# Optimization experiments

Hardware: AMD Instinct MI355X
Metric: run time of the kernel (lower is better)

The kernel has to match this reference:

```python
import jax, jax.numpy as jnp
import numpy as np

B, CIN, L, D, H, DK, DV, K, KE = 8, 16, 256, 256, 8, 32, 32, 3, 5
EPS = 1e-9

def r2c(p):
    return p[..., 0] + 1j * p[..., 1]

def c2r(z):
    return jnp.stack([jnp.real(z), jnp.imag(z)], axis=-1)

def conv1d(x, w):
    # x: [B,C,L] complex, w: [O,C,Kt] complex, 'same' padding (pad = K//2)
    kt = w.shape[-1]; pad = kt // 2; Lx = x.shape[-1]
    xp = jnp.pad(x, ((0, 0), (0, 0), (pad, pad)))
    return sum(jnp.einsum('bcl,oc->bol', xp[:, :, i:i + Lx], w[:, :, i]) for i in range(kt))

def eca(x, w):
    # Efficient Channel Attention (complex): global avg pool over length,
    # 1D conv (kernel KE) across channels, split sigmoid gate, rescale.
    C = x.shape[1]; pad = w.shape[0] // 2
    y = x.mean(axis=-1)                              # [B,C] complex
    yp = jnp.pad(y, ((0, 0), (pad, pad)))
    z = sum(w[i] * yp[:, i:i + C] for i in range(w.shape[0]))
    a = jax.nn.sigmoid(z.real) + 1j * jax.nn.sigmoid(z.imag)
    return x * a[:, :, None]

def magminmax(s):
    # MagMinMaxNorm: min-max normalize magnitudes along last dim, keep phase.
    mag = jnp.abs(s)
    mn = mag.min(axis=-1, keepdims=True)
    mx = mag.max(axis=-1, keepdims=True)
    return s * (((mag - mn) / (mx - mn + EPS)) / (mag + EPS))

def mha(qi, ki, vi, Wq, Wk, Wv, Wo):
    # qi/ki/vi: [B, L, D] complex
    b, lq, _ = qi.shape
    q = jnp.einsum('bld,de->ble', qi, Wq).reshape(b, lq, H, DK)
    k = jnp.einsum('bld,de->ble', ki, Wk).reshape(b, -1, H, DK)
    v = jnp.einsum('bld,de->ble', vi, Wv).reshape(b, -1, H, DV)
    s = jnp.einsum('bqhd,bkhd->bhqk', q, k) * (1.0 / DK ** 0.5)
    o = jnp.einsum('bhqk,bkhd->bqhd', magminmax(s), v).reshape(b, lq, H * DV)
    return jnp.einsum('ble,ed->bld', o, Wo)

def ssca(A, Bx, Wq, Wk, Wv, Wo, eca_w, conv_w):
    # A, Bx: [B, D, L] complex. Wq/Wk/Wv/Wo indexed [AA, BB, AB, BA].
    At = jnp.swapaxes(A, 1, 2)
    Bt = jnp.swapaxes(Bx, 1, 2)
    Waa = mha(At, At, At, Wq[0], Wk[0], Wv[0], Wo[0])
    Xbb = mha(Bt, Bt, Bt, Wq[1], Wk[1], Wv[1], Wo[1])
    Yab = mha(At, Bt, Bt, Wq[2], Wk[2], Wv[2], Wo[2])
    Zba = mha(Bt, At, At, Wq[3], Wk[3], Wv[3], Wo[3])
    # cat along sequence dim (dim=1 pre-transpose in torch), then back to [B, D, 4L]
    Xc = jnp.swapaxes(jnp.concatenate([Waa, Xbb, Yab, Zba], axis=1), 1, 2)
    return conv1d(eca(Xc, eca_w), conv_w)

def fusion(X1, X2, head_w, head_b, wq, wk, wv, wo, ssca_eca_w, ssca_conv_w, top_eca_w):
    X1c, X2c = r2c(X1), r2c(X2)
    hw, hb = r2c(head_w), r2c(head_b)
    Wq, Wk, Wv, Wo = r2c(wq), r2c(wk), r2c(wv), r2c(wo)
    se, sc, te = r2c(ssca_eca_w), r2c(ssca_conv_w), r2c(top_eca_w)
    A = conv1d(X1c, hw[0]) + hb[0][None, :, None]
    Bc = conv1d(X2c, hw[1]) + hb[1][None, :, None]
    R = ssca(A, Bc, Wq[0], Wk[0], Wv[0], Wo[0], se[0], sc[0])
    kk = ssca(jnp.fft.ifft(A, axis=-1), jnp.fft.ifft(Bc, axis=-1),
              Wq[1], Wk[1], Wv[1], Wo[1], se[1], sc[1])
    R2 = jnp.concatenate([R, jnp.fft.fft(kk, axis=-1)], axis=1)      # [B, 2D, 4L]
    k2 = jnp.concatenate([kk, jnp.fft.ifft(R2[:, :D], axis=-1)], axis=1)
    return eca(R2, te[0]), eca(k2, te[1])

def setup_inputs() -> dict:
    key = jax.random.key(0)
    ks = jax.random.split(key, 11)
    def rn(k, shape, s=1.0):
        return jax.random.normal(k, shape, dtype=jnp.float32) * s
    wscale = 1.0 / D ** 0.5
    return {
        'X1': rn(ks[0], (B, CIN, L, 2)),
        'X2': rn(ks[1], (B, CIN, L, 2)),
        'head_w': rn(ks[2], (2, D, CIN, K, 2), 0.1),
        'head_b': rn(ks[3], (2, D, 2), 0.1),
        'wq': rn(ks[4], (2, 4, D, H * DK, 2), wscale),
        'wk': rn(ks[5], (2, 4, D, H * DK, 2), wscale),
        'wv': rn(ks[6], (2, 4, D, H * DV, 2), wscale),
        'wo': rn(ks[7], (2, 4, H * DV, D, 2), wscale),
        'ssca_eca_w': rn(ks[8], (2, KE, 2), 0.3),
        'ssca_conv_w': rn(ks[9], (2, D, D, K, 2), wscale),
        'top_eca_w': rn(ks[10], (2, KE, 2), 0.3),
    }

def reference(X1, X2, head_w, head_b, wq, wk, wv, wo, ssca_eca_w, ssca_conv_w, top_eca_w):
    Rc, kc = fusion(X1, X2, head_w, head_b, wq, wk, wv, wo, ssca_eca_w, ssca_conv_w, top_eca_w)
    return c2r(Rc), c2r(kc)
```

## Files before the change

kernel.cpp:

```cpp
#include <hip/hip_runtime.h>
#include <math.h>

namespace {

constexpr int Bn = 8, CINn = 16, Ln = 256, Dn = 256, Hn = 8, DKn = 32, DVn = 32;
constexpr int KWn = 3, KEn = 5, L4n = 1024;
constexpr float EPSf = 1e-9f;
constexpr int XP = 1040;
constexpr int LP = 40;

typedef __attribute__((ext_vector_type(8))) short short8b;
typedef __attribute__((ext_vector_type(4))) float f32x4;

__device__ __forceinline__ float2 cmul(float2 a, float2 b){
  return make_float2(a.x*b.x - a.y*b.y, a.x*b.y + a.y*b.x);
}
__device__ __forceinline__ float2 cfma(float2 a, float2 b, float2 c){
  c.x = fmaf(a.x, b.x, c.x); c.x = fmaf(-a.y, b.y, c.x);
  c.y = fmaf(a.x, b.y, c.y); c.y = fmaf(a.y, b.x, c.y);
  return c;
}
__device__ __forceinline__ ushort f2bf(float f){
  uint u = __float_as_uint(f);
  u += 0x7fffu + ((u >> 16) & 1u);
  return (ushort)(u >> 16);
}
__device__ __forceinline__ uint cvt_pk_bf16(float a, float b){
  uint u;
  asm("v_cvt_pk_bf16_f32 %0, %1, %2" : "=v"(u) : "v"(a), "v"(b));
  return u;
}
__device__ __forceinline__ short8b neg8(short8b v){
  union { short8b s; uint u[4]; } x; x.s = v;
  #pragma unroll
  for (int i = 0; i < 4; ++i) x.u[i] ^= 0x80008000u;
  return x.s;
}

__global__ void head_conv_kernel(const float2* __restrict__ X, const float2* __restrict__ hw,
                                 const float2* __restrict__ hb, float2* __restrict__ out){
  int idx = blockIdx.x * blockDim.x + threadIdx.x;
  if (idx >= Bn*Dn*Ln) return;
  int l = idx & (Ln-1);
  int o = (idx >> 8) & (Dn-1);
  int b = idx >> 16;
  float2 acc = hb[o];
  for (int c = 0; c < CINn; ++c){
    const float2* xr = X + (size_t)(b*CINn + c)*Ln;
    const float2* wr = hw + (size_t)(o*CINn + c)*KWn;
    #pragma unroll
    for (int i = 0; i < KWn; ++i){
      int ll = l + i - 1;
      if (ll >= 0 && ll < Ln) acc = cfma(xr[ll], wr[i], acc);
    }
  }
  out[idx] = acc;
}

template<int N, int LOG>
__global__ void fft_rows_kernel(const float2* __restrict__ src0, float2* __restrict__ dst0,
                                int schans, int scoff, int dchans, int dcoff,
                                float sign, float scale, float2* __restrict__ ysum){
  __shared__ float2 buf[N];
  __shared__ float2 tw[N/2];
  __shared__ float rx[256], ry[256];
  int row = blockIdx.x;
  int rb = row >> 8, rc = row & 255;
  const float2* src = src0 + (size_t)(rb*schans + scoff + rc)*N;
  float2* dst = dst0 + (size_t)(rb*dchans + dcoff + rc)*N;
  int tid = threadIdx.x;
  for (int i = tid; i < N/2; i += 256){
    float a = sign * 6.2831853071795864f * (float)i / (float)N;
    float s, c; __sincosf(a, &s, &c);
    tw[i] = make_float2(c, s);
  }
  for (int i = tid; i < N; i += 256){
    unsigned r = __brev((unsigned)i) >> (32 - LOG);
    buf[r] = src[i];
  }
  __syncthreads();
  for (int st = 1; st <= LOG; ++st){
    int half = 1 << (st-1);
    for (int bf = tid; bf < N/2; bf += 256){
      int blk = bf >> (st-1);
      int pos = bf & (half-1);
      int i0 = (blk << st) + pos;
      int i1 = i0 + half;
      float2 w = tw[pos << (LOG-st)];
      float2 u = buf[i0];
      float2 t = cmul(w, buf[i1]);
      buf[i0] = make_float2(u.x + t.x, u.y + t.y);
      buf[i1] = make_float2(u.x - t.x, u.y - t.y);
    }
    __syncthreads();
  }
  float sx = 0.f, sy = 0.f;
  for (int i = tid; i < N; i += 256){
    float2 o = make_float2(buf[i].x * scale, buf[i].y * scale);
    dst[i] = o; sx += o.x; sy += o.y;
  }
  if (ysum){
    rx[tid] = sx; ry[tid] = sy; __syncthreads();
    for (int st = 128; st > 0; st >>= 1){
      if (tid < st){ rx[tid] += rx[tid+st]; ry[tid] += ry[tid+st]; }
      __syncthreads();
    }
    if (tid == 0)
      ysum[(size_t)rb*dchans + dcoff + rc] = make_float2(rx[0]*(1.f/N), ry[0]*(1.f/N));
  }
}

__global__ void row_mean_map(const float2* __restrict__ src0, int schans, int scoff,
                             float2* __restrict__ y, int dchans, int dcoff){
  int row = blockIdx.x;
  int rb = row >> 8, rc = row & 255;
  const float2* xr = src0 + (size_t)(rb*schans + scoff + rc)*L4n;
  int tid = threadIdx.x;
  float sx = 0.f, sy = 0.f;
  for (int i = tid; i < L4n; i += 256){ float2 v = xr[i]; sx += v.x; sy += v.y; }
  __shared__ float rx[256], ry[256];
  rx[tid] = sx; ry[tid] = sy; __syncthreads();
  for (int st = 128; st > 0; st >>= 1){
    if (tid < st){ rx[tid] += rx[tid+st]; ry[tid] += ry[tid+st]; }
    __syncthreads();
  }
  if (tid == 0)
    y[(size_t)rb*dchans + dcoff + rc] = make_float2(rx[0]*(1.f/L4n), ry[0]*(1.f/L4n));
}

__device__ __forceinline__ void cgemm_core(
    const ushort* __restrict__ Are, const ushort* __restrict__ Aim, int pitchA, int am0,
    const ushort* __restrict__ Bre, const ushort* __restrict__ Bim, int pitchB, int n0,
    int K, int conv, float2* __restrict__ cbase, size_t crow, int cmode,
    ushort* __restrict__ ore, ushort* __restrict__ oim)
{
  __shared__ ushort sh[16896];
  ushort* As_re = sh;
  ushort* As_im = sh + 5120;
  ushort* Bs_re = sh + 10240;
  ushort* Bs_im = sh + 12800;
  int tid = threadIdx.x;
  int lane = tid & 63, w = tid >> 6;
  int lrow = lane & 15, lhalf = lane >> 4;
  f32x4 ar[2][4], ai[2][4];
  #pragma unroll
  for (int s = 0; s < 2; ++s)
    #pragma unroll
    for (int t = 0; t < 4; ++t){ ar[s][t] = (f32x4){0,0,0,0}; ai[s][t] = (f32x4){0,0,0,0}; }
  int nk = K >> 5;
  for (int kc = 0; kc < nk; ++kc){
    int k0 = kc << 5;
    __syncthreads();
    #pragma unroll
    for (int rep = 0; rep < 4; ++rep){
      int q = tid + rep*256;
      int row = q >> 3, kq = (q & 7)*4;
      size_t go = (size_t)(am0 + row)*pitchA + k0 + kq;
      *(uint2*)&As_re[row*LP + kq] = *(const uint2*)&Are[go];
      *(uint2*)&As_im[row*LP + kq] = *(const uint2*)&Aim[go];
    }
    if (!conv){
      #pragma unroll
      for (int rep = 0; rep < 2; ++rep){
        int q = tid + rep*256;
        int row = q >> 3, kq = (q & 7)*4;
        size_t go = (size_t)(n0 + row)*pitchB + k0 + kq;
        *(uint2*)&Bs_re[row*LP + kq] = *(const uint2*)&Bre[go];
        *(uint2*)&Bs_im[row*LP + kq] = *(const uint2*)&Bim[go];
      }
    } else {
      #pragma unroll
      for (int rep = 0; rep < 8; ++rep){
        int idx = tid + rep*256;
        int k = idx >> 6, nn = idx & 63;
        uint kk = (uint)(k0 + k);
        uint c = (kk * 0xAAABu) >> 17;
        int i = (int)(kk - c*3u);
        size_t go = (size_t)c*XP + 8 + n0 + nn + i - 1;
        Bs_re[nn*LP + k] = Bre[go];
        Bs_im[nn*LP + k] = Bim[go];
      }
    }
    __syncthreads();
    short8b afr[2], afi[2], bfr[4], bfi[4];
    #pragma unroll
    for (int s = 0; s < 2; ++s){
      int row = w*32 + s*16 + lrow;
      afr[s] = *(const short8b*)&As_re[row*LP + lhalf*8];
      afi[s] = *(const short8b*)&As_im[row*LP + lhalf*8];
    }
    #pragma unroll
    for (int t = 0; t < 4; ++t){
      int row = t*16 + lrow;
      bfr[t] = *(const short8b*)&Bs_re[row*LP + lhalf*8];
      bfi[t] = *(const short8b*)&Bs_im[row*LP + lhalf*8];
    }
    #pragma unroll
    for (int s = 0; s < 2; ++s){
      short8b ain = neg8(afi[s]);
      #pragma unroll
      for (int t = 0; t < 4; ++t){
        ar[s][t] = __builtin_amdgcn_mfma_f32_16x16x32_bf16(ain,    bfi[t], ar[s][t], 0, 0, 0);
        ar[s][t] = __builtin_amdgcn_mfma_f32_16x16x32_bf16(afr[s], bfr[t], ar[s][t], 0, 0, 0);
        ai[s][t] = __builtin_amdgcn_mfma_f32_16x16x32_bf16(afi[s], bfr[t], ai[s][t], 0, 0, 0);
        ai[s][t] = __builtin_amdgcn_mfma_f32_16x16x32_bf16(afr[s], bfi[t], ai[s][t], 0, 0, 0);
      }
    }
  }
  if (cmode == 0){
    #pragma unroll
    for (int s = 0; s < 2; ++s)
      #pragma unroll
      for (int t = 0; t < 4; ++t)
        #pragma unroll
        for (int r = 0; r < 4; ++r){
          int mm = w*32 + s*16 + lhalf*4 + r;
          int nn = t*16 + lrow;
          if (ore){
            ore[(size_t)mm*crow + nn] = f2bf(ar[s][t][r]);
            oim[(size_t)mm*crow + nn] = f2bf(ai[s][t][r]);
          } else {
            cbase[(size_t)mm*crow + nn] = make_float2(ar[s][t][r], ai[s][t][r]);
          }
        }
  } else {
    float2* T = (float2*)sh;
    #pragma unroll
    for (int h2 = 0; h2 < 2; ++h2){
      __syncthreads();
      #pragma unroll
      for (int s = 0; s < 2; ++s)
        #pragma unroll
        for (int t2 = 0; t2 < 2; ++t2){
          int t = h2*2 + t2;
          #pragma unroll
          for (int r = 0; r < 4; ++r){
            int mm = w*32 + s*16 + lhalf*4 + r;
            int nn = t2*16 + lrow;
            T[mm*33 + nn] = make_float2(ar[s][t][r], ai[s][t][r]);
          }
        }
      __syncthreads();
      #pragma unroll
      for (int rep = 0; rep < 16; ++rep){
        int idx = tid + rep*256;
        int mm = idx & 127, nn = idx >> 7;
        float2 v = T[mm*33 + nn];
        if (ore){
          ore[(size_t)(h2*32 + nn)*crow + mm] = f2bf(v.x);
          oim[(size_t)(h2*32 + nn)*crow + mm] = f2bf(v.y);
        } else {
          cbase[(size_t)(h2*32 + nn)*crow + mm] = v;
        }
      }
    }
  }
}

__global__ __launch_bounds__(256) void qkv_mfma(
    const ushort* __restrict__ aAre, const ushort* __restrict__ aAim,
    const ushort* __restrict__ aBre, const ushort* __restrict__ aBim,
    const ushort* __restrict__ WqRe, const ushort* __restrict__ WqIm,
    const ushort* __restrict__ WkRe, const ushort* __restrict__ WkIm,
    const ushort* __restrict__ WvRe, const ushort* __restrict__ WvIm,
    ushort* __restrict__ QpRe, ushort* __restrict__ QpIm,
    ushort* __restrict__ KpRe, ushort* __restrict__ KpIm,
    ushort* __restrict__ VpRe, ushort* __restrict__ VpIm,
    int set, int m0, size_t pstride)
{
  int my = blockIdx.y;
  int ml = my / 3, which = my - ml*3;
  int m = m0 + ml;
  bool useA = (which == 0) ? (m == 0 || m == 2) : (m == 0 || m == 3);
  const ushort* Are = useA ? aAre : aBre;
  const ushort* Aim = useA ? aAim : aBim;
  const ushort* WRe = (which == 0) ? WqRe : (which == 1) ? WkRe : WvRe;
  const ushort* WIm = (which == 0) ? WqIm : (which == 1) ? WkIm : WvIm;
  size_t woff = (size_t)(set*4 + m)*Dn*Dn;
  int bx = blockIdx.x;
  int nt = bx & 3, mt = (bx >> 2) & 1, b = bx >> 3;
  int l0 = mt*128, e0 = nt*64;
  const ushort* ARe = Are + (size_t)b*Ln*Dn;
  const ushort* AIm = Aim + (size_t)b*Ln*Dn;
  size_t po = (size_t)ml*pstride;
  if (which == 2){
    ushort* orp = VpRe + po + ((size_t)b*Dn + e0)*Ln + l0;
    ushort* oip = VpIm + po + ((size_t)b*Dn + e0)*Ln + l0;
    cgemm_core(ARe, AIm, Dn, l0, WRe + woff, WIm + woff, Dn, e0, Dn, 0,
               nullptr, Ln, 1, orp, oip);
  } else {
    ushort* orp = ((which == 0) ? QpRe : KpRe) + po + ((size_t)b*Ln + l0)*Dn + e0;
    ushort* oip = ((which == 0) ? QpIm : KpIm) + po + ((size_t)b*Ln + l0)*Dn + e0;
    cgemm_core(ARe, AIm, Dn, l0, WRe + woff, WIm + woff, Dn, e0, Dn, 0,
               nullptr, Dn, 0, orp, oip);
  }
}

__global__ __launch_bounds__(256) void wo_mfma(
    const ushort* __restrict__ ORe, const ushort* __restrict__ OIm,
    const ushort* __restrict__ WoRe, const ushort* __restrict__ WoIm,
    float2* __restrict__ Xc, int set, int m0)
{
  int ml = blockIdx.y;
  int m = m0 + ml;
  size_t woff = (size_t)(set*4 + m)*Dn*Dn;
  int bx = blockIdx.x;
  int nt = bx & 3, mt = (bx >> 2) & 1, b = bx >> 3;
  int l0 = mt*128, d0 = nt*64;
  const ushort* ARe = ORe + ((size_t)ml*Bn + b)*Ln*Dn;
  const ushort* AIm = OIm + ((size_t)ml*Bn + b)*Ln*Dn;
  float2* cb = Xc + ((size_t)b*Dn + d0)*L4n + m*Ln + l0;
  cgemm_core(ARe, AIm, Dn, l0, WoRe + woff, WoIm + woff, Dn, d0, Dn, 0,
             cb, L4n, 1, nullptr, nullptr);
}

__global__ __launch_bounds__(256) void conv_mfma(
    const ushort* __restrict__ WRe, const ushort* __restrict__ WIm,
    const ushort* __restrict__ XRe, const ushort* __restrict__ XIm,
    float2* __restrict__ out, int ochans)
{
  int bx = blockIdx.x;
  int xt = bx & 15, ot = (bx >> 4) & 1, b = bx >> 5;
  int o0 = ot*128, x0 = xt*64;
  const ushort* xr = XRe + (size_t)b*Dn*XP;
  const ushort* xi = XIm + (size_t)b*Dn*XP;
  float2* cb = out + ((size_t)(b*ochans) + o0)*L4n + x0;
  cgemm_core(WRe, WIm, 768, o0, xr, xi, XP, x0, 768, 1, cb, L4n, 0,
             nullptr, nullptr);
}

__global__ __launch_bounds__(256) void attn_mfma(
    const ushort* __restrict__ QRe, const ushort* __restrict__ QIm,
    const ushort* __restrict__ KRe, const ushort* __restrict__ KIm,
    const ushort* __restrict__ VRe, const ushort* __restrict__ VIm,
    ushort* __restrict__ ORe, ushort* __restrict__ OIm, size_t pstride)
{
  size_t po = (size_t)blockIdx.y*pstride;
  const ushort* qre = QRe + po; const ushort* qim = QIm + po;
  const ushort* kre = KRe + po; const ushort* kim = KIm + po;
  const ushort* vre = VRe + po; const ushort* vim = VIm + po;
  ushort* ore = ORe + po; ushort* oim = OIm + po;
  int bx = blockIdx.x;
  int qt = bx >> 6, h = (bx >> 3) & 7, b = bx & 7;
  int q0 = qt*16;
  int tid = threadIdx.x;
  int lane = tid & 63, w = tid >> 6;
  int lg = lane >> 4, lr = lane & 15;
  __shared__ float4 shm4[1056];
  __shared__ float2 mmb[4][4][4];
  ushort* PsRe = (ushort*)shm4;
  ushort* PsIm = PsRe + 4224;
  float2* redbuf = (float2*)shm4;
  const float scl = 0.17677669529663687f;

  size_t qoff = ((size_t)(b*Ln + q0 + lr))*Dn + h*DKn + lg*8;
  short8b aqr = *(const short8b*)&qre[qoff];
  short8b aqi = *(const short8b*)&qim[qoff];
  short8b aqin = neg8(aqi);

  f32x4 sr[4], si[4];
  #pragma unroll
  for (int t = 0; t < 4; ++t){ sr[t] = (f32x4){0,0,0,0}; si[t] = (f32x4){0,0,0,0}; }
  #pragma unroll
  for (int t = 0; t < 4; ++t){
    int kcol = w*64 + t*16 + lr;
    size_t koff = ((size_t)(b*Ln + kcol))*Dn + h*DKn + lg*8;
    short8b bkr = *(const short8b*)&kre[koff];
    short8b bki = *(const short8b*)&kim[koff];
    sr[t] = __builtin_amdgcn_mfma_f32_16x16x32_bf16(aqin, bki, sr[t], 0, 0, 0);
    sr[t] = __builtin_amdgcn_mfma_f32_16x16x32_bf16(aqr,  bkr, sr[t], 0, 0, 0);
    si[t] = __builtin_amdgcn_mfma_f32_16x16x32_bf16(aqi,  bkr, si[t], 0, 0, 0);
    si[t] = __builtin_amdgcn_mfma_f32_16x16x32_bf16(aqr,  bki, si[t], 0, 0, 0);
  }
  float s2a[4][4];
  float mn2[4], mx2[4];
  #pragma unroll
  for (int r = 0; r < 4; ++r){ mn2[r] = 3.4e38f; mx2[r] = 0.f; }
  #pragma unroll
  for (int t = 0; t < 4; ++t)
    #pragma unroll
    for (int r = 0; r < 4; ++r){
      float x = sr[t][r]*scl, y = si[t][r]*scl;
      sr[t][r] = x; si[t][r] = y;
      float s2 = fmaf(x, x, y*y);
      s2a[t][r] = s2;
      mn2[r] = fminf(mn2[r], s2); mx2[r] = fmaxf(mx2[r], s2);
    }
  #pragma unroll
  for (int off = 1; off < 16; off <<= 1)
    #pragma unroll
    for (int r = 0; r < 4; ++r){
      mn2[r] = fminf(mn2[r], __shfl_xor(mn2[r], off));
      mx2[r] = fmaxf(mx2[r], __shfl_xor(mx2[r], off));
    }
  if (lr == 0){
    #pragma unroll
    for (int r = 0; r < 4; ++r) mmb[w][lg][r] = make_float2(mn2[r], mx2[r]);
  }
  __syncthreads();
  float mnv[4], invr[4];
  #pragma unroll
  for (int r = 0; r < 4; ++r){
    float2 v0 = mmb[0][lg][r], v1 = mmb[1][lg][r];
    float2 v2 = mmb[2][lg][r], v3 = mmb[3][lg][r];
    float fmn2 = fminf(fminf(v0.x, v1.x), fminf(v2.x, v3.x));
    float fmx2 = fmaxf(fmaxf(v0.y, v1.y), fmaxf(v2.y, v3.y));
    mnv[r] = sqrtf(fmn2);
    invr[r] = __builtin_amdgcn_rcpf(sqrtf(fmx2) - mnv[r] + EPSf);
  }
  #pragma unroll
  for (int t = 0; t < 4; ++t)
    #pragma unroll
    for (int r = 0; r < 4; ++r){
      int q = lg*4 + r, k = w*64 + t*16 + lr;
      float m = sqrtf(s2a[t][r]);
      float f = (m - mnv[r])*invr[r]*__builtin_amdgcn_rcpf(m + EPSf);
      uint u = cvt_pk_bf16(sr[t][r]*f, si[t][r]*f);
      PsRe[q*264 + k] = (ushort)u;
      PsIm[q*264 + k] = (ushort)(u >> 16);
    }
  f32x4 pr[2], pi[2];
  #pragma unroll
  for (int t = 0; t < 2; ++t){ pr[t] = (f32x4){0,0,0,0}; pi[t] = (f32x4){0,0,0,0}; }
  #pragma unroll
  for (int kc = 0; kc < 2; ++kc){
    int k0 = w*64 + kc*32;
    short8b par = *(const short8b*)&PsRe[lr*264 + k0 + lg*8];
    short8b pai = *(const short8b*)&PsIm[lr*264 + k0 + lg*8];
    short8b pain = neg8(pai);
    #pragma unroll
    for (int t = 0; t < 2; ++t){
      int dv = t*16 + lr;
      size_t voff = ((size_t)(b*Dn + h*DVn + dv))*Ln + k0 + lg*8;
      short8b bvr = *(const short8b*)&vre[voff];
      short8b bvi = *(const short8b*)&vim[voff];
      pr[t] = __builtin_amdgcn_mfma_f32_16x16x32_bf16(pain, bvi, pr[t], 0, 0, 0);
      pr[t] = __builtin_amdgcn_mfma_f32_16x16x32_bf16(par,  bvr, pr[t], 0, 0, 0);
      pi[t] = __builtin_amdgcn_mfma_f32_16x16x32_bf16(pai,  bvr, pi[t], 0, 0, 0);
      pi[t] = __builtin_amdgcn_mfma_f32_16x16x32_bf16(par,  bvi, pi[t], 0, 0, 0);
    }
  }
  __syncthreads();
  #pragma unroll
  for (int t = 0; t < 2; ++t)
    #pragma unroll
    for (int r = 0; r < 4; ++r)
      redbuf[(w*16 + lg*4 + r)*32 + t*16 + lr] = make_float2(pr[t][r], pi[t][r]);
  __syncthreads();
  #pragma unroll
  for (int rep = 0; rep < 2; ++rep){
    int idx = tid + rep*256;
    int q = idx >> 5, dv = idx & 31;
    float2 s0 = redbuf[(0*16 + q)*32 + dv], s1 = redbuf[(1*16 + q)*32 + dv];
    float2 s2 = redbuf[(2*16 + q)*32 + dv], s3 = redbuf[(3*16 + q)*32 + dv];
    float sx = s0.x + s1.x + s2.x + s3.x;
    float sy = s0.y + s1.y + s2.y + s3.y;
    size_t oo = ((size_t)(b*Ln + q0 + q))*Dn + h*DVn + dv;
    uint u = cvt_pk_bf16(sx, sy);
    ore[oo] = (ushort)u; oim[oo] = (ushort)(u >> 16);
  }
}

__global__ void pack_at(const float2* __restrict__ in, ushort* __restrict__ ore,
                        ushort* __restrict__ oim){
  __shared__ float2 T[32][33];
  int bx = blockIdx.x;
  int lt = bx & 7, dt = (bx >> 3) & 7, b = bx >> 6;
  int tid = threadIdx.x;
  int c = tid & 31, rr = tid >> 5;
  #pragma unroll
  for (int it = 0; it < 4; ++it){
    int d = rr + it*8;
    T[d][c] = in[((size_t)b*Dn + dt*32 + d)*Ln + lt*32 + c];
  }
  __syncthreads();
  #pragma unroll
  for (int it = 0; it < 4; ++it){
    int l = rr + it*8;
    float2 v = T[c][l];
    size_t o = ((size_t)b*Ln + lt*32 + l)*Dn + dt*32 + c;
    ore[o] = f2bf(v.x); oim[o] = f2bf(v.y);
  }
}

__global__ void pack_wt(const float2* __restrict__ wq, const float2* __restrict__ wk,
                        const float2* __restrict__ wv, const float2* __restrict__ wo,
                        ushort* r0, ushort* i0, ushort* r1, ushort* i1,
                        ushort* r2, ushort* i2, ushort* r3, ushort* i3){
  int f = blockIdx.y;
  const float2* in = (f == 0) ? wq : (f == 1) ? wk : (f == 2) ? wv : wo;
  ushort* orr = (f == 0) ? r0 : (f == 1) ? r1 : (f == 2) ? r2 : r3;
  ushort* oii = (f == 0) ? i0 : (f == 1) ? i1 : (f == 2) ? i2 : i3;
  int bx = blockIdx.x;
  int tile = bx & 63, mat = bx >> 6;
  int kt = tile & 7, nt = tile >> 3;
  __shared__ float2 T[32][33];
  int tid = threadIdx.x;
  int c = tid & 31, rr = tid >> 5;
  #pragma unroll
  for (int it = 0; it < 4; ++it){
    int k = rr + it*8;
    T[k][c] = in[((size_t)(mat*256 + kt*32 + k))*256 + nt*32 + c];
  }
  __syncthreads();
  #pragma unroll
  for (int it = 0; it < 4; ++it){
    int n = rr + it*8;
    float2 v = T[c][n];
    size_t o = ((size_t)(mat*256 + nt*32 + n))*256 + kt*32 + c;
    orr[o] = f2bf(v.x); oii[o] = f2bf(v.y);
  }
}

__global__ void pack_sc(const float2* __restrict__ sc, ushort* __restrict__ ore,
                        ushort* __restrict__ oim){
  size_t idx = (size_t)blockIdx.x*256 + threadIdx.x;
  float2 v = sc[idx];
  ore[idx] = f2bf(v.x); oim[idx] = f2bf(v.y);
}

__global__ void eca_apply_pack(const float2* __restrict__ X, const float2* __restrict__ g,
                               ushort* __restrict__ xre, ushort* __restrict__ xim){
  int idx = blockIdx.x*256 + threadIdx.x;
  int row = idx >> 10, x = idx & 1023;
  float2 v = cmul(X[idx], g[row]);
  size_t o = (size_t)row*XP + 8 + x;
  xre[o] = f2bf(v.x); xim[o] = f2bf(v.y);
  if (x < 8){ size_t o2 = (size_t)row*XP + x; xre[o2] = 0; xim[o2] = 0; }
  if (x >= 1016){ size_t o2 = (size_t)row*XP + x + 16; xre[o2] = 0; xim[o2] = 0; }
}

__global__ void eca_gate_kernel(const float2* __restrict__ y, const float2* __restrict__ w,
                                float2* __restrict__ g, int C){
  int idx = blockIdx.x*blockDim.x + threadIdx.x;
  if (idx >= Bn*C) return;
  int c = idx % C;
  int b = idx / C;
  float2 z = make_float2(0.f, 0.f);
  #pragma unroll
  for (int i = 0; i < KEn; ++i){
    int cc = c + i - 2;
    if (cc >= 0 && cc < C) z = cfma(w[i], y[b*C + cc], z);
  }
  g[idx] = make_float2(1.f/(1.f + expf(-z.x)), 1.f/(1.f + expf(-z.y)));
}

__global__ void eca_apply4(float4* __restrict__ X, const float2* __restrict__ g){
  int idx = blockIdx.x*256 + threadIdx.x;
  int row = idx >> 9;
  float2 gg = g[row];
  float4 v = X[idx];
  float2 a = cmul(make_float2(v.x, v.y), gg);
  float2 b = cmul(make_float2(v.z, v.w), gg);
  X[idx] = make_float4(a.x, a.y, b.x, b.y);
}

}

extern "C" void kernel_launch(void* const* d_in, const int* in_sizes, int n_in,
                              void* d_out, int out_size, void* d_ws, size_t ws_size,
                              hipStream_t stream){
  const float2* X1 = (const float2*)d_in[0];
  const float2* X2 = (const float2*)d_in[1];
  const float2* head_w = (const float2*)d_in[2];
  const float2* head_b = (const float2*)d_in[3];
  const float2* wq = (const float2*)d_in[4];
  const float2* wk = (const float2*)d_in[5];
  const float2* wv = (const float2*)d_in[6];
  const float2* wo = (const float2*)d_in[7];
  const float2* se = (const float2*)d_in[8];
  const float2* sc = (const float2*)d_in[9];
  const float2* te = (const float2*)d_in[10];

  const size_t SZ_BDL = (size_t)Bn*Dn*Ln;
  const size_t SZ_X   = (size_t)Bn*Dn*L4n;
  const size_t NAt    = (size_t)Bn*Ln*Dn;

  const size_t US_FIX = 2*(4*NAt) + 2*(4*8*(size_t)65536)
                      + 2*(2*(size_t)Dn*768) + 2*((size_t)Bn*Dn*XP);
  auto need_bytes = [&](int mc){
    return ((size_t)4*SZ_BDL + SZ_X + 32768)*sizeof(float2)
         + (US_FIX + (size_t)8*mc*NAt)*sizeof(ushort);
  };
  int mcount = 1;
  if (ws_size >= need_bytes(4)) mcount = 4;
  else if (ws_size >= need_bytes(2)) mcount = 2;

  float2* p = (float2*)d_ws;
  float2* A  = p;  p += SZ_BDL;
  float2* Bc = p;  p += SZ_BDL;
  float2* iA = p;  p += SZ_BDL;
  float2* iB = p;  p += SZ_BDL;
  float2* Xc = p;  p += SZ_X;
  float2* ybufX = p; p += (size_t)Bn*Dn;
  float2* ybufR = p; p += (size_t)Bn*2*Dn;
  float2* ybufK = p; p += (size_t)Bn*2*Dn;
  float2* gbuf  = p; p += (size_t)Bn*2*Dn;

  ushort* us = (ushort*)p;
  auto grab = [&](size_t n){ ushort* r = us; us += n; return r; };
  ushort *AtRe[4], *AtIm[4];
  for (int i = 0; i < 4; ++i){ AtRe[i] = grab(NAt); AtIm[i] = grab(NAt); }
  ushort *WRe4[4], *WIm4[4];
  for (int f = 0; f < 4; ++f){ WRe4[f] = grab(8*(size_t)65536); WIm4[f] = grab(8*(size_t)65536); }
  ushort* ScRe = grab(2*(size_t)Dn*768);
  ushort* ScIm = grab(2*(size_t)Dn*768);
  ushort* XRe = grab((size_t)Bn*Dn*XP);
  ushort* XIm = grab((size_t)Bn*Dn*XP);
  ushort* QpRe = grab((size_t)mcount*NAt);
  ushort* QpIm = grab((size_t)mcount*NAt);
  ushort* KpRe = grab((size_t)mcount*NAt);
  ushort* KpIm = grab((size_t)mcount*NAt);
  ushort* VpRe = grab((size_t)mcount*NAt);
  ushort* VpIm = grab((size_t)mcount*NAt);
  ushort* ObRe = grab((size_t)mcount*NAt);
  ushort* ObIm = grab((size_t)mcount*NAt);

  float2* out0 = (float2*)d_out;
  float2* out1 = out0 + (size_t)Bn*2*Dn*L4n;

  head_conv_kernel<<<(Bn*Dn*Ln)/256, 256, 0, stream>>>(X1, head_w, head_b, A);
  head_conv_kernel<<<(Bn*Dn*Ln)/256, 256, 0, stream>>>(
      X2, head_w + (size_t)Dn*CINn*KWn, head_b + Dn, Bc);

  fft_rows_kernel<256,8><<<Bn*Dn, 256, 0, stream>>>(A,  iA, 256,0,256,0, 1.0f, 1.0f/256.0f, nullptr);
  fft_rows_kernel<256,8><<<Bn*Dn, 256, 0, stream>>>(Bc, iB, 256,0,256,0, 1.0f, 1.0f/256.0f, nullptr);

  pack_at<<<512, 256, 0, stream>>>(A,  AtRe[0], AtIm[0]);
  pack_at<<<512, 256, 0, stream>>>(Bc, AtRe[1], AtIm[1]);
  pack_at<<<512, 256, 0, stream>>>(iA, AtRe[2], AtIm[2]);
  pack_at<<<512, 256, 0, stream>>>(iB, AtRe[3], AtIm[3]);
  pack_wt<<<dim3(512, 4), 256, 0, stream>>>(wq, wk, wv, wo,
      WRe4[0], WIm4[0], WRe4[1], WIm4[1], WRe4[2], WIm4[2], WRe4[3], WIm4[3]);
  pack_sc<<<1536, 256, 0, stream>>>(sc, ScRe, ScIm);

  auto run_ssca = [&](int ia, int ib, int set, float2* dstbase, float2* ybufT){
    for (int m0 = 0; m0 < 4; m0 += mcount){
      qkv_mfma<<<dim3(64, 3*mcount), 256, 0, stream>>>(
          AtRe[ia], AtIm[ia], AtRe[ib], AtIm[ib],
          WRe4[0], WIm4[0], WRe4[1], WIm4[1], WRe4[2], WIm4[2],
          QpRe, QpIm, KpRe, KpIm, VpRe, VpIm, set, m0, NAt);
      attn_mfma<<<dim3(Bn*Hn*16, mcount), 256, 0, stream>>>(
          QpRe, QpIm, KpRe, KpIm, VpRe, VpIm, ObRe, ObIm, NAt);
      wo_mfma<<<dim3(64, mcount), 256, 0, stream>>>(
          ObRe, ObIm, WRe4[3], WIm4[3], Xc, set, m0);
    }
    row_mean_map<<<Bn*Dn, 256, 0, stream>>>(Xc, Dn, 0, ybufX, Dn, 0);
    eca_gate_kernel<<<(Bn*Dn + 255)/256, 256, 0, stream>>>(ybufX, se + set*KEn, gbuf, Dn);
    eca_apply_pack<<<(int)(SZ_X/256), 256, 0, stream>>>(Xc, gbuf, XRe, XIm);
    conv_mfma<<<256, 256, 0, stream>>>(
        ScRe + (size_t)set*Dn*768, ScIm + (size_t)set*Dn*768, XRe, XIm, dstbase, 2*Dn);
    row_mean_map<<<Bn*Dn, 256, 0, stream>>>(dstbase, 2*Dn, 0, ybufT, 2*Dn, 0);
  };

  run_ssca(0, 1, 0, out0, ybufR);
  run_ssca(2, 3, 1, out1, ybufK);

  fft_rows_kernel<1024,10><<<Bn*Dn, 256, 0, stream>>>(out1, out0, 2*Dn,0, 2*Dn,Dn, -1.0f, 1.0f, ybufR);
  fft_rows_kernel<1024,10><<<Bn*Dn, 256, 0, stream>>>(out0, out1, 2*Dn,0, 2*Dn,Dn, 1.0f, 1.0f/1024.0f, ybufK);

  eca_gate_kernel<<<(Bn*2*Dn + 255)/256, 256, 0, stream>>>(ybufR, te, gbuf, 2*Dn);
  eca_apply4<<<(int)((size_t)Bn*2*Dn*L4n/2/256), 256, 0, stream>>>((float4*)out0, gbuf);
  eca_gate_kernel<<<(Bn*2*Dn + 255)/256, 256, 0, stream>>>(ybufK, te + KEn, gbuf, 2*Dn);
  eca_apply4<<<(int)((size_t)Bn*2*Dn*L4n/2/256), 256, 0, stream>>>((float4*)out1, gbuf);
}
```

Baseline: 419.9 us.

## Give each wave a full 16-query row block in attention, removing cross-wave reductions

The attention kernel previously split the 256 keys across four waves for one 16-query tile. That required LDS min/max exchange, block barriers and an LDS reduction of partial outputs. Now each wave owns 16 queries and processes all 256 keys itself, keeping 16 score tiles in registers. It computes normalized scores in 32-key chunks into a small per-wave LDS buffer and writes outputs directly, and the grid shrinks fourfold. This removes barriers and the reduction, at the cost of much higher register pressure (32 f32x4 accumulators), which can lower occupancy and cause spills.

```diff
diff --git a/kernel.cpp b/kernel.cpp
--- a/kernel.cpp
+++ b/kernel.cpp
@@ -341,16 +341,14 @@
   const ushort* vre = VRe + po; const ushort* vim = VIm + po;
   ushort* ore = ORe + po; ushort* oim = OIm + po;
   int bx = blockIdx.x;
-  int qt = bx >> 6, h = (bx >> 3) & 7, b = bx & 7;
-  int q0 = qt*16;
+  int qt2 = bx >> 6, h = (bx >> 3) & 7, b = bx & 7;
   int tid = threadIdx.x;
   int lane = tid & 63, w = tid >> 6;
   int lg = lane >> 4, lr = lane & 15;
-  __shared__ float4 shm4[1056];
-  __shared__ float2 mmb[4][4][4];
-  ushort* PsRe = (ushort*)shm4;
-  ushort* PsIm = PsRe + 4224;
-  float2* redbuf = (float2*)shm4;
+  int q0 = qt2*64 + w*16;
+  __shared__ ushort Ps[4][2][16][40];
+  ushort* psr = &Ps[w][0][0][0];
+  ushort* psi = &Ps[w][1][0][0];
   const float scl = 0.17677669529663687f;
 
   size_t qoff = ((size_t)(b*Ln + q0 + lr))*Dn + h*DKn + lg*8;
@@ -358,12 +356,12 @@
   short8b aqi = *(const short8b*)&qim[qoff];
   short8b aqin = neg8(aqi);
 
-  f32x4 sr[4], si[4];
-  #pragma unroll
-  for (int t = 0; t < 4; ++t){ sr[t] = (f32x4){0,0,0,0}; si[t] = (f32x4){0,0,0,0}; }
-  #pragma unroll
-  for (int t = 0; t < 4; ++t){
-    int kcol = w*64 + t*16 + lr;
+  f32x4 sr[16], si[16];
+  #pragma unroll
+  for (int t = 0; t < 16; ++t){ sr[t] = (f32x4){0,0,0,0}; si[t] = (f32x4){0,0,0,0}; }
+  #pragma unroll
+  for (int t = 0; t < 16; ++t){
+    int kcol = t*16 + lr;
     size_t koff = ((size_t)(b*Ln + kcol))*Dn + h*DKn + lg*8;
     short8b bkr = *(const short8b*)&kre[koff];
     short8b bki = *(const short8b*)&kim[koff];
@@ -372,18 +370,16 @@
     si[t] = __builtin_amdgcn_mfma_f32_16x16x32_bf16(aqi,  bkr, si[t], 0, 0, 0);
     si[t] = __builtin_amdgcn_mfma_f32_16x16x32_bf16(aqr,  bki, si[t], 0, 0, 0);
   }
-  float s2a[4][4];
   float mn2[4], mx2[4];
   #pragma unroll
   for (int r = 0; r < 4; ++r){ mn2[r] = 3.4e38f; mx2[r] = 0.f; }
   #pragma unroll
-  for (int t = 0; t < 4; ++t)
+  for (int t = 0; t < 16; ++t)
     #pragma unroll
     for (int r = 0; r < 4; ++r){
       float x = sr[t][r]*scl, y = si[t][r]*scl;
       sr[t][r] = x; si[t][r] = y;
       float s2 = fmaf(x, x, y*y);
-      s2a[t][r] = s2;
       mn2[r] = fminf(mn2[r], s2); mx2[r] = fmaxf(mx2[r], s2);
     }
   #pragma unroll
@@ -393,45 +389,39 @@
       mn2[r] = fminf(mn2[r], __shfl_xor(mn2[r], off));
       mx2[r] = fmaxf(mx2[r], __shfl_xor(mx2[r], off));
     }
-  if (lr == 0){
-    #pragma unroll
-    for (int r = 0; r < 4; ++r) mmb[w][lg][r] = make_float2(mn2[r], mx2[r]);
-  }
-  __syncthreads();
   float mnv[4], invr[4];
   #pragma unroll
   for (int r = 0; r < 4; ++r){
-    float2 v0 = mmb[0][lg][r], v1 = mmb[1][lg][r];
-    float2 v2 = mmb[2][lg][r], v3 = mmb[3][lg][r];
-    float fmn2 = fminf(fminf(v0.x, v1.x), fminf(v2.x, v3.x));
-    float fmx2 = fmaxf(fmaxf(v0.y, v1.y), fmaxf(v2.y, v3.y));
-    mnv[r] = sqrtf(fmn2);
-    invr[r] = __builtin_amdgcn_rcpf(sqrtf(fmx2) - mnv[r] + EPSf);
-  }
-  #pragma unroll
-  for (int t = 0; t < 4; ++t)
-    #pragma unroll
-    for (int r = 0; r < 4; ++r){
-      int q = lg*4 + r, k = w*64 + t*16 + lr;
-      float m = sqrtf(s2a[t][r]);
-      float f = (m - mnv[r])*invr[r]*__builtin_amdgcn_rcpf(m + EPSf);
-      uint u = cvt_pk_bf16(sr[t][r]*f, si[t][r]*f);
-      PsRe[q*264 + k] = (ushort)u;
-      PsIm[q*264 + k] = (ushort)(u >> 16);
-    }
+    mnv[r] = sqrtf(mn2[r]);
+    invr[r] = __builtin_amdgcn_rcpf(sqrtf(mx2[r]) - mnv[r] + EPSf);
+  }
   f32x4 pr[2], pi[2];
   #pragma unroll
   for (int t = 0; t < 2; ++t){ pr[t] = (f32x4){0,0,0,0}; pi[t] = (f32x4){0,0,0,0}; }
   #pragma unroll
-  for (int kc = 0; kc < 2; ++kc){
-    int k0 = w*64 + kc*32;
-    short8b par = *(const short8b*)&PsRe[lr*264 + k0 + lg*8];
-    short8b pai = *(const short8b*)&PsIm[lr*264 + k0 + lg*8];
+  for (int ch = 0; ch < 8; ++ch){
+    #pragma unroll
+    for (int j = 0; j < 2; ++j){
+      int kt = ch*2 + j;
+      #pragma unroll
+      for (int r = 0; r < 4; ++r){
+        int q = lg*4 + r;
+        float x = sr[kt][r], y = si[kt][r];
+        float s2 = fmaf(x, x, y*y);
+        float m = sqrtf(s2);
+        float f = (m - mnv[r])*invr[r]*__builtin_amdgcn_rcpf(m + EPSf);
+        uint u = cvt_pk_bf16(x*f, y*f);
+        psr[q*40 + j*16 + lr] = (ushort)u;
+        psi[q*40 + j*16 + lr] = (ushort)(u >> 16);
+      }
+    }
+    short8b par = *(const short8b*)&psr[lr*40 + lg*8];
+    short8b pai = *(const short8b*)&psi[lr*40 + lg*8];
     short8b pain = neg8(pai);
     #pragma unroll
     for (int t = 0; t < 2; ++t){
       int dv = t*16 + lr;
-      size_t voff = ((size_t)(b*Dn + h*DVn + dv))*Ln + k0 + lg*8;
+      size_t voff = ((size_t)(b*Dn + h*DVn + dv))*Ln + ch*32 + lg*8;
       short8b bvr = *(const short8b*)&vre[voff];
       short8b bvi = *(const short8b*)&vim[voff];
       pr[t] = __builtin_amdgcn_mfma_f32_16x16x32_bf16(pain, bvi, pr[t], 0, 0, 0);
@@ -440,25 +430,15 @@
       pi[t] = __builtin_amdgcn_mfma_f32_16x16x32_bf16(par,  bvi, pi[t], 0, 0, 0);
     }
   }
-  __syncthreads();
   #pragma unroll
   for (int t = 0; t < 2; ++t)
     #pragma unroll
-    for (int r = 0; r < 4; ++r)
-      redbuf[(w*16 + lg*4 + r)*32 + t*16 + lr] = make_float2(pr[t][r], pi[t][r]);
-  __syncthreads();
-  #pragma unroll
-  for (int rep = 0; rep < 2; ++rep){
-    int idx = tid + rep*256;
-    int q = idx >> 5, dv = idx & 31;
-    float2 s0 = redbuf[(0*16 + q)*32 + dv], s1 = redbuf[(1*16 + q)*32 + dv];
-    float2 s2 = redbuf[(2*16 + q)*32 + dv], s3 = redbuf[(3*16 + q)*32 + dv];
-    float sx = s0.x + s1.x + s2.x + s3.x;
-    float sy = s0.y + s1.y + s2.y + s3.y;
-    size_t oo = ((size_t)(b*Ln + q0 + q))*Dn + h*DVn + dv;
-    uint u = cvt_pk_bf16(sx, sy);
-    ore[oo] = (ushort)u; oim[oo] = (ushort)(u >> 16);
-  }
+    for (int r = 0; r < 4; ++r){
+      int q = q0 + lg*4 + r, dv = t*16 + lr;
+      size_t oo = ((size_t)(b*Ln + q))*Dn + h*DVn + dv;
+      uint u = cvt_pk_bf16(pr[t][r], pi[t][r]);
+      ore[oo] = (ushort)u; oim[oo] = (ushort)(u >> 16);
+    }
 }
 
 __global__ void pack_at(const float2* __restrict__ in, ushort* __restrict__ ore,
@@ -640,7 +620,7 @@
           AtRe[ia], AtIm[ia], AtRe[ib], AtIm[ib],
           WRe4[0], WIm4[0], WRe4[1], WIm4[1], WRe4[2], WIm4[2],
           QpRe, QpIm, KpRe, KpIm, VpRe, VpIm, set, m0, NAt);
-      attn_mfma<<<dim3(Bn*Hn*16, mcount), 256, 0, stream>>>(
+      attn_mfma<<<dim3(Bn*Hn*4, mcount), 256, 0, stream>>>(
           QpRe, QpIm, KpRe, KpIm, VpRe, VpIm, ObRe, ObIm, NAt);
       wo_mfma<<<dim3(64, mcount), 256, 0, stream>>>(
           ObRe, ObIm, WRe4[3], WIm4[3], Xc, set, m0);
```

Result: slower. 448.8 us (+6.9%).
